# Kernel tuning notes

Hardware: AMD Instinct MI355X
Metric: run time of the kernel (lower is better)

## Reference

```python
import jax, jax.numpy as jnp
import numpy as np

HEADS = 8
HEAD_DIM = 64
WINDOW = 65  # odd


def setup_inputs() -> dict:
    key = jax.random.key(0)
    k1, k2, k3 = jax.random.split(key, 3)
    B, S, D_MODEL = 2, 2048, HEADS * HEAD_DIM
    x = jax.random.normal(k1, (B, S, D_MODEL), dtype=jnp.float32)
    W_qkv = jax.random.normal(k2, (D_MODEL, 3 * HEADS * HEAD_DIM), dtype=jnp.float32) * (1.0 / np.sqrt(D_MODEL))
    W_out = jax.random.normal(k3, (HEADS * HEAD_DIM, D_MODEL), dtype=jnp.float32) * (1.0 / np.sqrt(HEADS * HEAD_DIM))
    b_out = jnp.zeros((D_MODEL,), dtype=jnp.float32)
    return {"x": x, "W_qkv": W_qkv, "W_out": W_out, "b_out": b_out}


def reference(x, W_qkv, W_out, b_out):
    B, S, _ = x.shape
    H, D, W = HEADS, HEAD_DIM, WINDOW
    pad = W // 2

    qkv = x @ W_qkv                              # [B,S,3*H*D]
    qkv = qkv.reshape(B, S, H, 3 * D)
    q, k, v = jnp.split(qkv, 3, axis=-1)          # each [B,S,H,D]

    # zero-pad along sequence (matches tf.pad; padded keys get score 0, NOT -inf)
    k_pad = jnp.pad(k, ((0, 0), (pad, pad), (0, 0), (0, 0)))
    v_pad = jnp.pad(v, ((0, 0), (pad, pad), (0, 0), (0, 0)))

    # sliding windows via gather: [S, W] indices into padded seq (= tf.signal.frame)
    idx = jnp.arange(S)[:, None] + jnp.arange(W)[None, :]
    k_win = k_pad[:, idx]                         # [B,S,W,H,D]
    v_win = v_pad[:, idx]                         # [B,S,W,H,D]

    scale = 1.0 / jnp.sqrt(jnp.asarray(D, dtype=x.dtype))
    scores = jnp.einsum('bshd,bswhd->bhsw', q, k_win) * scale  # [B,H,S,W]
    weights = jax.nn.softmax(scores, axis=-1)
    attn = jnp.einsum('bhsw,bswhd->bshd', weights, v_win)       # [B,S,H,D]
    attn = attn.reshape(B, S, H * D)
    return attn @ W_out + b_out
```

## Files before the change

### kernel.cpp

```cpp
#include <hip/hip_runtime.h>
#include <hip/hip_bf16.h>
#include <stdint.h>

typedef short short8 __attribute__((ext_vector_type(8)));
typedef float f32x4 __attribute__((ext_vector_type(4)));
typedef unsigned short ushort4_t __attribute__((ext_vector_type(4)));
typedef unsigned short ushort8_t __attribute__((ext_vector_type(8)));

#define S_LEN 2048
#define NQKV 1536
#define DMODEL 512

__device__ inline unsigned short f2bf(float f) {
  unsigned int u = __float_as_uint(f);
  unsigned int r = (u + 0x7FFFu + ((u >> 16) & 1u)) >> 16;
  return (unsigned short)r;
}

__device__ __forceinline__ void gll16(const unsigned short* g, unsigned short* l) {
  __builtin_amdgcn_global_load_lds(
      (const __attribute__((address_space(1))) unsigned int*)g,
      (__attribute__((address_space(3))) unsigned int*)l, 16, 0, 0);
}

__global__ __launch_bounds__(256) void k_prep(const float* __restrict__ x,
                                              unsigned short* __restrict__ xb,
                                              const float* __restrict__ w1,
                                              unsigned short* __restrict__ o1,
                                              const float* __restrict__ w2,
                                              unsigned short* __restrict__ o2,
                                              unsigned short* __restrict__ Kp,
                                              unsigned short* __restrict__ Vp) {
  __shared__ float T[32][33];
  int bid = blockIdx.x;
  int t = threadIdx.x;
  if (bid < 1024) {
    int i = (bid * 256 + t) * 8;
    float4 a = *(const float4*)(x + i);
    float4 b = *(const float4*)(x + i + 4);
    ushort8_t o;
    o[0] = f2bf(a.x); o[1] = f2bf(a.y); o[2] = f2bf(a.z); o[3] = f2bf(a.w);
    o[4] = f2bf(b.x); o[5] = f2bf(b.y); o[6] = f2bf(b.z); o[7] = f2bf(b.w);
    *(ushort8_t*)(xb + i) = o;
    return;
  }
  if (bid >= 2048) {
    int p = bid - 2048;
    ushort8_t z = {};
    if (p < 16) {
      unsigned short* dst = Kp + (size_t)p * 2112 * 64;
#pragma unroll
      for (int i = 0; i < 2; i++) {
        int s = t + 256 * i;
        int row = s >> 3, c = s & 7;
        int r2 = row < 32 ? row : row - 32 + 2080;
        *(ushort8_t*)&dst[r2 * 64 + c * 8] = z;
      }
    } else {
      unsigned short* dst = Vp + (size_t)(p - 16) * 64 * 2112;
#pragma unroll
      for (int i = 0; i < 2; i++) {
        int s = t + 256 * i;
        int d = s >> 3, side = (s >> 2) & 1, c = s & 3;
        *(ushort8_t*)&dst[(size_t)d * 2112 + side * 2080 + c * 8] = z;
      }
    }
    return;
  }
  bid -= 1024;
  int bx = bid & 63, byy = bid >> 6;
  const float* w; unsigned short* o; int cols;
  if (bx < 48) { w = w1; o = o1; cols = 1536; }
  else         { w = w2; o = o2; cols = 512; bx -= 48; }
  int r0 = byy * 32, c0 = bx * 32;
  int tr = t / 32, tc = t % 32;
#pragma unroll
  for (int i = 0; i < 4; i++) {
    int r = tr + i * 8;
    T[r][tc] = w[(size_t)(r0 + r) * cols + c0 + tc];
  }
  __syncthreads();
#pragma unroll
  for (int i = 0; i < 4; i++) {
    int rr = tr + i * 8;
    o[(size_t)(c0 + rr) * 512 + r0 + tc] = f2bf(T[tc][rr]);
  }
}

__global__ __launch_bounds__(128) void k_gemm1(const unsigned short* __restrict__ A,
                                               const unsigned short* __restrict__ Bt,
                                               unsigned short* __restrict__ qs,
                                               unsigned short* __restrict__ kp,
                                               unsigned short* __restrict__ vp) {
  __shared__ __align__(16) unsigned short smem[24576];
  const int ASZ = 128 * 64, BOFF = 2 * 128 * 64, BSZ = 64 * 64;
  const int t = threadIdx.x, lane = t & 63, wid = t >> 6;
  const int m0 = blockIdx.y * 128, n0 = blockIdx.x * 64;
  const int wm = wid * 64;
  const int lr = lane & 15, lg = lane >> 4;
  const unsigned short* Ab = A + (size_t)m0 * 512;
  const unsigned short* Bb = Bt + (size_t)n0 * 512;
  f32x4 acc[4][4] = {};

  auto stage = [&](int buf, int kt) {
#pragma unroll
    for (int c = 0; c < 8; c++) {
      int f = t + 128 * c;
      int row = f >> 3, ch = f & 7;
      gll16(Ab + (size_t)row * 512 + kt + ((ch ^ (row & 7)) << 3),
            &smem[buf * ASZ + f * 8]);
    }
#pragma unroll
    for (int c = 0; c < 4; c++) {
      int f = t + 128 * c;
      int row = f >> 3, ch = f & 7;
      gll16(Bb + (size_t)row * 512 + kt + ((ch ^ (row & 7)) << 3),
            &smem[BOFF + buf * BSZ + f * 8]);
    }
  };

  stage(0, 0);
  int buf = 0;
  for (int it = 0; it < 8; ++it) {
    __syncthreads();
    if (it + 1 < 8) stage(buf ^ 1, (it + 1) * 64);
    const unsigned short* Ap = &smem[buf * ASZ];
    const unsigned short* Bp = &smem[BOFF + buf * BSZ];
#pragma unroll
    for (int sl = 0; sl < 2; sl++) {
      const int cs = sl * 4 + lg;
      short8 af[4], bfv[4];
#pragma unroll
      for (int i = 0; i < 4; i++) {
        int row = wm + i * 16 + lr;
        af[i] = *(const short8*)&Ap[row * 64 + ((cs ^ (row & 7)) << 3)];
      }
#pragma unroll
      for (int i = 0; i < 4; i++) {
        int row = i * 16 + lr;
        bfv[i] = *(const short8*)&Bp[row * 64 + ((cs ^ (row & 7)) << 3)];
      }
#pragma unroll
      for (int mi = 0; mi < 4; mi++)
#pragma unroll
        for (int ni = 0; ni < 4; ni++)
          acc[mi][ni] = __builtin_amdgcn_mfma_f32_16x16x32_bf16(af[mi], bfv[ni], acc[mi][ni], 0, 0, 0);
    }
    buf ^= 1;
  }

  __syncthreads();
#pragma unroll
  for (int mi = 0; mi < 4; mi++)
#pragma unroll
    for (int ni = 0; ni < 4; ni++)
#pragma unroll
      for (int j = 0; j < 4; j++) {
        int row = wm + mi * 16 + lg * 4 + j;
        int col = ni * 16 + lr;
        smem[row * 64 + (((col >> 3) ^ ((row >> 3) & 7)) << 3) + (col & 7)] =
            f2bf(acc[mi][ni][j]);
      }
  __syncthreads();

  const int b_ = m0 >> 11;
  const int posb = m0 & 2047;
  const int h = n0 / 192, seg = (n0 % 192) >> 6;
  if (seg < 2) {
    unsigned short* dst = (seg == 0)
        ? qs + ((size_t)(b_ * 8 + h) * 2048 + posb) * 64
        : kp + ((size_t)(b_ * 8 + h) * 2112 + 32 + posb) * 64;
#pragma unroll
    for (int i = 0; i < 8; i++) {
      int s = t + 128 * i;
      int row = s >> 3, ch = s & 7;
      int src = row * 64 + ((ch ^ ((row >> 3) & 7)) << 3);
      *(ushort8_t*)&dst[s * 8] = *(const ushort8_t*)&smem[src];
    }
  } else {
    unsigned short* dst = vp + (size_t)(b_ * 8 + h) * 64 * 2112;
#pragma unroll
    for (int i = 0; i < 8; i++) {
      int s = t + 128 * i;
      int dl = s >> 4, pc = s & 15;
      ushort8_t v;
#pragma unroll
      for (int j = 0; j < 8; j++) {
        int row = pc * 8 + j;
        v[j] = smem[row * 64 + ((((dl >> 3) ^ (pc & 7)) << 3)) + (dl & 7)];
      }
      *(ushort8_t*)&dst[(size_t)dl * 2112 + 32 + posb + pc * 8] = v;
    }
  }
}

template <int BM, int BN>
__global__ __launch_bounds__(256) void k_gemm(const unsigned short* __restrict__ A,
                                              const unsigned short* __restrict__ Bt,
                                              float* __restrict__ Cout,
                                              const float* __restrict__ bias,
                                              int M, int N, int K) {
  constexpr int MR = BM / 32, NR = BN / 32;
  constexpr int CA = BM / 32, CB = BN / 32;
  constexpr int STAGE_SH = 2 * (BM + BN) * 64;
  constexpr int BOUNCE_SH = BM * BN * 2;
  constexpr int SMEM_SH = STAGE_SH > BOUNCE_SH ? STAGE_SH : BOUNCE_SH;
  __shared__ __align__(16) unsigned short smem[SMEM_SH];
  const int ASZ = BM * 64, BOFF = 2 * BM * 64, BSZ = BN * 64;

  const int t = threadIdx.x, lane = t & 63, wid = t >> 6;
  const int m0 = blockIdx.y * BM, n0 = blockIdx.x * BN;
  const int wm = (wid >> 1) * (BM / 2), wn = (wid & 1) * (BN / 2);
  const int lr = lane & 15, lg = lane >> 4;
  const unsigned short* Ab = A + (size_t)m0 * K;
  const unsigned short* Bb = Bt + (size_t)n0 * K;
  f32x4 acc[MR][NR] = {};

  const int NT = K / 64;
  auto stage = [&](int buf, int kt) {
#pragma unroll
    for (int c = 0; c < CA; c++) {
      int f = t + 256 * c;
      int row = f >> 3, ch = f & 7;
      gll16(Ab + (size_t)row * K + kt + ((ch ^ (row & 7)) << 3),
            &smem[buf * ASZ + f * 8]);
    }
#pragma unroll
    for (int c = 0; c < CB; c++) {
      int f = t + 256 * c;
      int row = f >> 3, ch = f & 7;
      gll16(Bb + (size_t)row * K + kt + ((ch ^ (row & 7)) << 3),
            &smem[BOFF + buf * BSZ + f * 8]);
    }
  };

  stage(0, 0);
  int buf = 0;
  for (int it = 0; it < NT; ++it) {
    __syncthreads();
    if (it + 1 < NT) stage(buf ^ 1, (it + 1) * 64);
    const unsigned short* Ap = &smem[buf * ASZ];
    const unsigned short* Bp = &smem[BOFF + buf * BSZ];
#pragma unroll
    for (int sl = 0; sl < 2; sl++) {
      const int cs = sl * 4 + lg;
      short8 af[MR], bfv[NR];
#pragma unroll
      for (int i = 0; i < MR; i++) {
        int row = wm + i * 16 + lr;
        af[i] = *(const short8*)&Ap[row * 64 + ((cs ^ (row & 7)) << 3)];
      }
#pragma unroll
      for (int i = 0; i < NR; i++) {
        int row = wn + i * 16 + lr;
        bfv[i] = *(const short8*)&Bp[row * 64 + ((cs ^ (row & 7)) << 3)];
      }
#pragma unroll
      for (int mi = 0; mi < MR; mi++)
#pragma unroll
        for (int ni = 0; ni < NR; ni++)
          acc[mi][ni] = __builtin_amdgcn_mfma_f32_16x16x32_bf16(af[mi], bfv[ni], acc[mi][ni], 0, 0, 0);
    }
    buf ^= 1;
  }

  __syncthreads();
  float* ft = (float*)smem;
#pragma unroll
  for (int mi = 0; mi < MR; mi++)
#pragma unroll
    for (int ni = 0; ni < NR; ni++)
#pragma unroll
      for (int j = 0; j < 4; j++)
        ft[(wm + mi * 16 + lg * 4 + j) * BN + wn + ni * 16 + lr] = acc[mi][ni][j];
  __syncthreads();
#pragma unroll
  for (int i = 0; i < BM * BN / 1024; i++) {
    int s = t + 256 * i;
    int row = s / (BN / 4), ch = s % (BN / 4);
    float4 v = *(const float4*)&ft[row * BN + ch * 4];
    float4 bv = *(const float4*)&bias[n0 + ch * 4];
    v.x += bv.x; v.y += bv.y; v.z += bv.z; v.w += bv.w;
    *(float4*)&Cout[(size_t)(m0 + row) * N + n0 + ch * 4] = v;
  }
}

__global__ __launch_bounds__(256) void k_attn(const unsigned short* __restrict__ Qs,
                                              const unsigned short* __restrict__ Kp,
                                              const unsigned short* __restrict__ Vp,
                                              unsigned short* __restrict__ attnb) {
  __shared__ __align__(16) unsigned short Kt[128 * 64];
  __shared__ __align__(16) unsigned short Vt[64 * 192];
  __shared__ __align__(16) unsigned short Qt[64 * 64];
  const int t = threadIdx.x, lane = t & 63, w = t >> 6;
  const int blk = blockIdx.x;
  const int sbi = blk & 31, h = (blk >> 5) & 7, b = blk >> 8;
  const int sb = sbi * 64;
  const int bh = b * 8 + h;
  const int lr = lane & 15, lg = lane >> 4;

  {
    const unsigned short* src = Kp + ((size_t)bh * 2112 + sb) * 64;
#pragma unroll
    for (int i = 0; i < 4; i++) {
      int s = t + 256 * i, row = s >> 3, c = s & 7;
      gll16(src + row * 64 + (c ^ (row & 7)) * 8, &Kt[s * 8]);
    }
  }
  {
    const unsigned short* src = Vp + (size_t)bh * 64 * 2112 + sb;
#pragma unroll
    for (int i = 0; i < 6; i++) {
      int s = t + 256 * i, d = s / 24, c = s - d * 24;
      gll16(src + (size_t)d * 2112 + (c ^ (d & 7)) * 8, &Vt[s * 8]);
    }
  }
  {
    const unsigned short* src = Qs + ((size_t)bh * 2048 + sb) * 64;
#pragma unroll
    for (int i = 0; i < 2; i++) {
      int s = t + 256 * i, row = s >> 3, c = s & 7;
      gll16(src + row * 64 + (c ^ (row & 7)) * 8, &Qt[s * 8]);
    }
  }
  __syncthreads();

  const int sw = (lr & 7) << 3;

  short8 qb[2];
#pragma unroll
  for (int ks = 0; ks < 2; ks++)
    qb[ks] = *(const short8*)&Qt[(w * 16 + lr) * 64 + ((ks * 32 + lg * 8) ^ sw)];

  f32x4 sc[5] = {};
#pragma unroll
  for (int ct = 0; ct < 5; ct++) {
#pragma unroll
    for (int ks = 0; ks < 2; ks++) {
      short8 ka = *(const short8*)&Kt[(w * 16 + ct * 16 + lr) * 64 + ((ks * 32 + lg * 8) ^ sw)];
      sc[ct] = __builtin_amdgcn_mfma_f32_16x16x32_bf16(ka, qb[ks], sc[ct], 0, 0, 0);
    }
  }

  float mx = -1e30f;
#pragma unroll
  for (int ct = 0; ct < 5; ct++)
#pragma unroll
    for (int j = 0; j < 4; j++) {
      int c2 = ct * 16 + lg * 4 + j;
      sc[ct][j] = (c2 >= lr && c2 <= lr + 64) ? sc[ct][j] * 0.125f : -1e30f;
      mx = fmaxf(mx, sc[ct][j]);
    }
  mx = fmaxf(mx, __shfl_xor(mx, 16, 64));
  mx = fmaxf(mx, __shfl_xor(mx, 32, 64));

  float pn[5][4];
  float sum = 0.0f;
#pragma unroll
  for (int ct = 0; ct < 5; ct++)
#pragma unroll
    for (int j = 0; j < 4; j++) {
      pn[ct][j] = __expf(sc[ct][j] - mx);
      sum += pn[ct][j];
    }
  sum += __shfl_xor(sum, 16, 64);
  sum += __shfl_xor(sum, 32, 64);
  float inv = 1.0f / sum;

  unsigned int w01[5], w23[5];
#pragma unroll
  for (int ct = 0; ct < 5; ct++) {
    w01[ct] = (unsigned int)f2bf(pn[ct][0] * inv) | ((unsigned int)f2bf(pn[ct][1] * inv) << 16);
    w23[ct] = (unsigned int)f2bf(pn[ct][2] * inv) | ((unsigned int)f2bf(pn[ct][3] * inv) << 16);
  }

  f32x4 oa[4] = {};
  const int h2 = lg & 1, tl = lg >> 1;
  const int sA = 32 * h2 + lr, sB = sA + 16;
#pragma unroll
  for (int ks = 0; ks < 3; ks++) {
    const int T0 = 2 * ks;
    const int T1 = (2 * ks + 1 < 5) ? (2 * ks + 1) : 4;
    unsigned int a0 = __shfl((int)w01[T0], sA, 64), a1 = __shfl((int)w23[T0], sA, 64);
    unsigned int a2 = __shfl((int)w01[T0], sB, 64), a3 = __shfl((int)w23[T0], sB, 64);
    unsigned int b0 = __shfl((int)w01[T1], sA, 64), b1 = __shfl((int)w23[T1], sA, 64);
    unsigned int b2 = __shfl((int)w01[T1], sB, 64), b3 = __shfl((int)w23[T1], sB, 64);
    union { unsigned int u[4]; short8 v; } pb;
    pb.u[0] = tl ? b0 : a0;
    pb.u[1] = tl ? b1 : a1;
    pb.u[2] = tl ? b2 : a2;
    pb.u[3] = tl ? b3 : a3;
    if (ks == 2 && tl) { pb.u[0] = 0; pb.u[1] = 0; pb.u[2] = 0; pb.u[3] = 0; }
    int pofl = w * 16 + ks * 32 + lg * 8;
#pragma unroll
    for (int nt = 0; nt < 4; nt++) {
      short8 va = *(const short8*)&Vt[(nt * 16 + lr) * 192 + (pofl ^ sw)];
      oa[nt] = __builtin_amdgcn_mfma_f32_16x16x32_bf16(va, pb.v, oa[nt], 0, 0, 0);
    }
  }

  const int s0 = sb + w * 16;
#pragma unroll
  for (int nt = 0; nt < 4; nt++) {
    ushort4_t o;
#pragma unroll
    for (int j = 0; j < 4; j++) o[j] = f2bf(oa[nt][j]);
    *(ushort4_t*)&attnb[((size_t)b * S_LEN + s0 + lr) * DMODEL + h * 64 + nt * 16 + lg * 4] = o;
  }
}

extern "C" void kernel_launch(void* const* d_in, const int* in_sizes, int n_in,
                              void* d_out, int out_size, void* d_ws, size_t ws_size,
                              hipStream_t stream) {
  const float* x    = (const float*)d_in[0];
  const float* Wqkv = (const float*)d_in[1];
  const float* Wout = (const float*)d_in[2];
  const float* bout = (const float*)d_in[3];
  char* ws = (char*)d_ws;
  unsigned short* xb    = (unsigned short*)(ws + 0);
  unsigned short* wqkvt = (unsigned short*)(ws + 4194304);
  unsigned short* woutt = (unsigned short*)(ws + 5767168);
  unsigned short* Qs    = (unsigned short*)(ws + 6291456);
  unsigned short* Kp    = (unsigned short*)(ws + 10485760);
  unsigned short* Vp    = (unsigned short*)(ws + 14811136);
  unsigned short* attnb = (unsigned short*)(ws + 19922944);

  hipLaunchKernelGGL(k_prep, dim3(2080), dim3(256), 0, stream,
                     x, xb, Wqkv, wqkvt, Wout, woutt, Kp, Vp);
  hipLaunchKernelGGL(k_gemm1, dim3(24, 32), dim3(128), 0, stream,
                     xb, wqkvt, Qs, Kp, Vp);
  hipLaunchKernelGGL(k_attn, dim3(512), dim3(256), 0, stream, Qs, Kp, Vp, attnb);
  hipLaunchKernelGGL((k_gemm<64, 64>), dim3(8, 64), dim3(256), 0, stream,
                     attnb, woutt, (float*)d_out, bout, 4096, 512, 512);
}
```

Baseline: 38.13 us.

## Fuse prep, QKV GEMM, attention and output GEMM into one cooperative kernel

Measured after the change: 145.5 us. 3.82x slower.

```diff
diff --git a/kernel.cpp b/kernel.cpp
--- a/kernel.cpp
+++ b/kernel.cpp
@@ -1,6 +1,9 @@
 #include <hip/hip_runtime.h>
 #include <hip/hip_bf16.h>
+#include <hip/hip_cooperative_groups.h>
 #include <stdint.h>
+
+namespace cg = cooperative_groups;
 
 typedef short short8 __attribute__((ext_vector_type(8)));
 typedef float f32x4 __attribute__((ext_vector_type(4)));
@@ -23,389 +26,396 @@
       (__attribute__((address_space(3))) unsigned int*)l, 16, 0, 0);
 }
 
-__global__ __launch_bounds__(256) void k_prep(const float* __restrict__ x,
-                                              unsigned short* __restrict__ xb,
-                                              const float* __restrict__ w1,
-                                              unsigned short* __restrict__ o1,
-                                              const float* __restrict__ w2,
-                                              unsigned short* __restrict__ o2,
-                                              unsigned short* __restrict__ Kp,
-                                              unsigned short* __restrict__ Vp) {
-  __shared__ float T[32][33];
-  int bid = blockIdx.x;
-  int t = threadIdx.x;
-  if (bid < 1024) {
-    int i = (bid * 256 + t) * 8;
-    float4 a = *(const float4*)(x + i);
-    float4 b = *(const float4*)(x + i + 4);
-    ushort8_t o;
-    o[0] = f2bf(a.x); o[1] = f2bf(a.y); o[2] = f2bf(a.z); o[3] = f2bf(a.w);
-    o[4] = f2bf(b.x); o[5] = f2bf(b.y); o[6] = f2bf(b.z); o[7] = f2bf(b.w);
-    *(ushort8_t*)(xb + i) = o;
-    return;
+__global__ __launch_bounds__(768, 3) void k_mega(
+    const float* __restrict__ x, const float* __restrict__ w1,
+    const float* __restrict__ w2, const float* __restrict__ bias,
+    unsigned short* __restrict__ xb, unsigned short* __restrict__ wqkvt,
+    unsigned short* __restrict__ woutt, unsigned short* __restrict__ Qs,
+    unsigned short* __restrict__ Kp, unsigned short* __restrict__ Vp,
+    unsigned short* __restrict__ attnb, float* __restrict__ out) {
+  __shared__ __align__(16) unsigned short smem[73728];
+  cg::grid_group grid = cg::this_grid();
+  const int blk = blockIdx.x;
+  const int t = threadIdx.x;
+  const int sub = t >> 8;
+  const int tl = t & 255;
+  const int lane = tl & 63, wid = tl >> 6;
+  const int lr = lane & 15, lg = lane >> 4;
+
+  {
+    float(*T)[33] = (float(*)[33])(smem + sub * 4096);
+    for (int it = 0; it < 3; ++it) {
+      int vb = blk * 3 + sub + it * 768;
+      int kind = (vb < 1024) ? 0 : (vb < 2048) ? 1 : (vb < 2080) ? 2 : -1;
+      const float* w = nullptr; unsigned short* o = nullptr;
+      int bx = 0, byy = 0, cols = 0;
+      if (kind == 0) {
+        int i = (vb * 256 + tl) * 8;
+        float4 a = *(const float4*)(x + i);
+        float4 b = *(const float4*)(x + i + 4);
+        ushort8_t ov;
+        ov[0] = f2bf(a.x); ov[1] = f2bf(a.y); ov[2] = f2bf(a.z); ov[3] = f2bf(a.w);
+        ov[4] = f2bf(b.x); ov[5] = f2bf(b.y); ov[6] = f2bf(b.z); ov[7] = f2bf(b.w);
+        *(ushort8_t*)(xb + i) = ov;
+      } else if (kind == 2) {
+        int p = vb - 2048;
+        ushort8_t z = {};
+        if (p < 16) {
+          unsigned short* dst = Kp + (size_t)p * 2112 * 64;
+#pragma unroll
+          for (int i = 0; i < 2; i++) {
+            int s = tl + 256 * i;
+            int row = s >> 3, c = s & 7;
+            int r2 = row < 32 ? row : row - 32 + 2080;
+            *(ushort8_t*)&dst[r2 * 64 + c * 8] = z;
+          }
+        } else {
+          unsigned short* dst = Vp + (size_t)(p - 16) * 64 * 2112;
+#pragma unroll
+          for (int i = 0; i < 2; i++) {
+            int s = tl + 256 * i;
+            int d = s >> 3, side = (s >> 2) & 1, c = s & 3;
+            *(ushort8_t*)&dst[(size_t)d * 2112 + side * 2080 + c * 8] = z;
+          }
+        }
+      } else if (kind == 1) {
+        int v2 = vb - 1024;
+        bx = v2 & 63; byy = v2 >> 6;
+        if (bx < 48) { w = w1; o = wqkvt; cols = 1536; }
+        else         { w = w2; o = woutt; cols = 512; bx -= 48; }
+        int r0 = byy * 32, c0 = bx * 32;
+        int tr = tl / 32, tc = tl % 32;
+#pragma unroll
+        for (int i = 0; i < 4; i++) {
+          int r = tr + i * 8;
+          T[r][tc] = w[(size_t)(r0 + r) * cols + c0 + tc];
+        }
+      }
+      __syncthreads();
+      if (kind == 1) {
+        int r0 = byy * 32, c0 = bx * 32;
+        int tr = tl / 32, tc = tl % 32;
+#pragma unroll
+        for (int i = 0; i < 4; i++) {
+          int rr = tr + i * 8;
+          o[(size_t)(c0 + rr) * 512 + r0 + tc] = f2bf(T[tc][rr]);
+        }
+      }
+      __syncthreads();
+    }
   }
-  if (bid >= 2048) {
-    int p = bid - 2048;
-    ushort8_t z = {};
-    if (p < 16) {
-      unsigned short* dst = Kp + (size_t)p * 2112 * 64;
+  grid.sync();
+
+  {
+    unsigned short* vs = smem + sub * 24576;
+    const int ASZ = 8192, BOFF = 16384, BSZ = 4096;
+    const int vb = blk * 3 + sub;
+    const int m0 = (vb / 24) * 128, n0 = (vb % 24) * 64;
+    const int wm = (wid >> 1) * 64, wn = (wid & 1) * 32;
+    const unsigned short* Ab = xb + (size_t)m0 * 512;
+    const unsigned short* Bb = wqkvt + (size_t)n0 * 512;
+    f32x4 acc[4][2] = {};
+
+    auto stage = [&](int buf, int kt) {
+#pragma unroll
+      for (int c = 0; c < 4; c++) {
+        int f = tl + 256 * c;
+        int row = f >> 3, ch = f & 7;
+        gll16(Ab + (size_t)row * 512 + kt + ((ch ^ (row & 7)) << 3),
+              &vs[buf * ASZ + f * 8]);
+      }
+#pragma unroll
+      for (int c = 0; c < 2; c++) {
+        int f = tl + 256 * c;
+        int row = f >> 3, ch = f & 7;
+        gll16(Bb + (size_t)row * 512 + kt + ((ch ^ (row & 7)) << 3),
+              &vs[BOFF + buf * BSZ + f * 8]);
+      }
+    };
+
+    stage(0, 0);
+    int buf = 0;
+    for (int it = 0; it < 8; ++it) {
+      __syncthreads();
+      if (it + 1 < 8) stage(buf ^ 1, (it + 1) * 64);
+      const unsigned short* Ap = &vs[buf * ASZ];
+      const unsigned short* Bp = &vs[BOFF + buf * BSZ];
+#pragma unroll
+      for (int sl = 0; sl < 2; sl++) {
+        const int cs = sl * 4 + lg;
+        short8 af[4], bfv[2];
+#pragma unroll
+        for (int i = 0; i < 4; i++) {
+          int row = wm + i * 16 + lr;
+          af[i] = *(const short8*)&Ap[row * 64 + ((cs ^ (row & 7)) << 3)];
+        }
+#pragma unroll
+        for (int i = 0; i < 2; i++) {
+          int row = wn + i * 16 + lr;
+          bfv[i] = *(const short8*)&Bp[row * 64 + ((cs ^ (row & 7)) << 3)];
+        }
+#pragma unroll
+        for (int mi = 0; mi < 4; mi++)
+#pragma unroll
+          for (int ni = 0; ni < 2; ni++)
+            acc[mi][ni] = __builtin_amdgcn_mfma_f32_16x16x32_bf16(af[mi], bfv[ni], acc[mi][ni], 0, 0, 0);
+      }
+      buf ^= 1;
+    }
+
+    __syncthreads();
+#pragma unroll
+    for (int mi = 0; mi < 4; mi++)
+#pragma unroll
+      for (int ni = 0; ni < 2; ni++)
+#pragma unroll
+        for (int j = 0; j < 4; j++) {
+          int row = wm + mi * 16 + lg * 4 + j;
+          int col = wn + ni * 16 + lr;
+          vs[row * 64 + (((col >> 3) ^ ((row >> 3) & 7)) << 3) + (col & 7)] =
+              f2bf(acc[mi][ni][j]);
+        }
+    __syncthreads();
+
+    const int b_ = m0 >> 11;
+    const int posb = m0 & 2047;
+    const int h = n0 / 192, seg = (n0 % 192) >> 6;
+    if (seg < 2) {
+      unsigned short* dst = (seg == 0)
+          ? Qs + ((size_t)(b_ * 8 + h) * 2048 + posb) * 64
+          : Kp + ((size_t)(b_ * 8 + h) * 2112 + 32 + posb) * 64;
+#pragma unroll
+      for (int i = 0; i < 4; i++) {
+        int s = tl + 256 * i;
+        int row = s >> 3, ch = s & 7;
+        int src = row * 64 + ((ch ^ ((row >> 3) & 7)) << 3);
+        *(ushort8_t*)&dst[s * 8] = *(const ushort8_t*)&vs[src];
+      }
+    } else {
+      unsigned short* dst = Vp + (size_t)(b_ * 8 + h) * 64 * 2112;
+#pragma unroll
+      for (int i = 0; i < 4; i++) {
+        int s = tl + 256 * i;
+        int dl = s >> 4, pc = s & 15;
+        ushort8_t v;
+#pragma unroll
+        for (int j = 0; j < 8; j++) {
+          int row = pc * 8 + j;
+          v[j] = vs[row * 64 + ((((dl >> 3) ^ (pc & 7)) << 3)) + (dl & 7)];
+        }
+        *(ushort8_t*)&dst[(size_t)dl * 2112 + 32 + posb + pc * 8] = v;
+      }
+    }
+  }
+  grid.sync();
+
+  {
+    unsigned short* Kt = smem;
+    unsigned short* Vt = smem + 12288;
+    unsigned short* Qt = smem + 28672;
+    const int h = blk & 7, sbi = (blk >> 3) & 15, b = blk >> 7;
+    const int sb = sbi * 128, bh = b * 8 + h;
+    const int w = t >> 6;
+    const int lane6 = t & 63;
+    const int alr = lane6 & 15, alg = lane6 >> 4;
+
+    {
+      const unsigned short* src = Kp + ((size_t)bh * 2112 + sb) * 64;
 #pragma unroll
       for (int i = 0; i < 2; i++) {
-        int s = t + 256 * i;
+        int s = t + 768 * i;
         int row = s >> 3, c = s & 7;
-        int r2 = row < 32 ? row : row - 32 + 2080;
-        *(ushort8_t*)&dst[r2 * 64 + c * 8] = z;
-      }
-    } else {
-      unsigned short* dst = Vp + (size_t)(p - 16) * 64 * 2112;
+        gll16(src + row * 64 + (c ^ (row & 7)) * 8, &Kt[s * 8]);
+      }
+    }
+    {
+      const unsigned short* src = Vp + (size_t)bh * 64 * 2112 + sb;
+#pragma unroll
+      for (int i = 0; i < 3; i++) {
+        int s = t + 768 * i;
+        if (s < 2048) {
+          int d = s >> 5, c = s & 31;
+          gll16(src + (size_t)d * 2112 + (c ^ (d & 7)) * 8, &Vt[s * 8]);
+        }
+      }
+    }
+    {
+      const unsigned short* src = Qs + ((size_t)bh * 2048 + sb) * 64;
 #pragma unroll
       for (int i = 0; i < 2; i++) {
-        int s = t + 256 * i;
-        int d = s >> 3, side = (s >> 2) & 1, c = s & 3;
-        *(ushort8_t*)&dst[(size_t)d * 2112 + side * 2080 + c * 8] = z;
-      }
-    }
-    return;
+        int s = t + 768 * i;
+        if (s < 1024) {
+          int row = s >> 3, c = s & 7;
+          gll16(src + row * 64 + (c ^ (row & 7)) * 8, &Qt[s * 8]);
+        }
+      }
+    }
+    __syncthreads();
+
+    if (w < 8) {
+      const int sw = (alr & 7) << 3;
+
+      short8 qb[2];
+#pragma unroll
+      for (int ks = 0; ks < 2; ks++)
+        qb[ks] = *(const short8*)&Qt[(w * 16 + alr) * 64 + ((ks * 32 + alg * 8) ^ sw)];
+
+      f32x4 sc[5] = {};
+#pragma unroll
+      for (int ct = 0; ct < 5; ct++) {
+#pragma unroll
+        for (int ks = 0; ks < 2; ks++) {
+          short8 ka = *(const short8*)&Kt[(w * 16 + ct * 16 + alr) * 64 + ((ks * 32 + alg * 8) ^ sw)];
+          sc[ct] = __builtin_amdgcn_mfma_f32_16x16x32_bf16(ka, qb[ks], sc[ct], 0, 0, 0);
+        }
+      }
+
+      float mx = -1e30f;
+#pragma unroll
+      for (int ct = 0; ct < 5; ct++)
+#pragma unroll
+        for (int j = 0; j < 4; j++) {
+          int c2 = ct * 16 + alg * 4 + j;
+          sc[ct][j] = (c2 >= alr && c2 <= alr + 64) ? sc[ct][j] * 0.125f : -1e30f;
+          mx = fmaxf(mx, sc[ct][j]);
+        }
+      mx = fmaxf(mx, __shfl_xor(mx, 16, 64));
+      mx = fmaxf(mx, __shfl_xor(mx, 32, 64));
+
+      float pn[5][4];
+      float sum = 0.0f;
+#pragma unroll
+      for (int ct = 0; ct < 5; ct++)
+#pragma unroll
+        for (int j = 0; j < 4; j++) {
+          pn[ct][j] = __expf(sc[ct][j] - mx);
+          sum += pn[ct][j];
+        }
+      sum += __shfl_xor(sum, 16, 64);
+      sum += __shfl_xor(sum, 32, 64);
+      float inv = 1.0f / sum;
+
+      unsigned int w01[5], w23[5];
+#pragma unroll
+      for (int ct = 0; ct < 5; ct++) {
+        w01[ct] = (unsigned int)f2bf(pn[ct][0] * inv) | ((unsigned int)f2bf(pn[ct][1] * inv) << 16);
+        w23[ct] = (unsigned int)f2bf(pn[ct][2] * inv) | ((unsigned int)f2bf(pn[ct][3] * inv) << 16);
+      }
+
+      f32x4 oa[4] = {};
+      const int h2 = alg & 1, tsel = alg >> 1;
+      const int sA = 32 * h2 + alr, sB = sA + 16;
+#pragma unroll
+      for (int ks = 0; ks < 3; ks++) {
+        const int T0 = 2 * ks;
+        const int T1 = (2 * ks + 1 < 5) ? (2 * ks + 1) : 4;
+        unsigned int a0 = __shfl((int)w01[T0], sA, 64), a1 = __shfl((int)w23[T0], sA, 64);
+        unsigned int a2 = __shfl((int)w01[T0], sB, 64), a3 = __shfl((int)w23[T0], sB, 64);
+        unsigned int b0 = __shfl((int)w01[T1], sA, 64), b1 = __shfl((int)w23[T1], sA, 64);
+        unsigned int b2 = __shfl((int)w01[T1], sB, 64), b3 = __shfl((int)w23[T1], sB, 64);
+        union { unsigned int u[4]; short8 v; } pb;
+        pb.u[0] = tsel ? b0 : a0;
+        pb.u[1] = tsel ? b1 : a1;
+        pb.u[2] = tsel ? b2 : a2;
+        pb.u[3] = tsel ? b3 : a3;
+        if (ks == 2 && tsel) { pb.u[0] = 0; pb.u[1] = 0; pb.u[2] = 0; pb.u[3] = 0; }
+        int pofl = w * 16 + ks * 32 + alg * 8;
+#pragma unroll
+        for (int nt = 0; nt < 4; nt++) {
+          short8 va = *(const short8*)&Vt[(nt * 16 + alr) * 256 + (pofl ^ sw)];
+          oa[nt] = __builtin_amdgcn_mfma_f32_16x16x32_bf16(va, pb.v, oa[nt], 0, 0, 0);
+        }
+      }
+
+      const int s0 = sb + w * 16;
+#pragma unroll
+      for (int nt = 0; nt < 4; nt++) {
+        ushort4_t o;
+#pragma unroll
+        for (int j = 0; j < 4; j++) o[j] = f2bf(oa[nt][j]);
+        *(ushort4_t*)&attnb[((size_t)b * S_LEN + s0 + alr) * DMODEL + h * 64 + nt * 16 + alg * 4] = o;
+      }
+    }
   }
-  bid -= 1024;
-  int bx = bid & 63, byy = bid >> 6;
-  const float* w; unsigned short* o; int cols;
-  if (bx < 48) { w = w1; o = o1; cols = 1536; }
-  else         { w = w2; o = o2; cols = 512; bx -= 48; }
-  int r0 = byy * 32, c0 = bx * 32;
-  int tr = t / 32, tc = t % 32;
-#pragma unroll
-  for (int i = 0; i < 4; i++) {
-    int r = tr + i * 8;
-    T[r][tc] = w[(size_t)(r0 + r) * cols + c0 + tc];
-  }
-  __syncthreads();
-#pragma unroll
-  for (int i = 0; i < 4; i++) {
-    int rr = tr + i * 8;
-    o[(size_t)(c0 + rr) * 512 + r0 + tc] = f2bf(T[tc][rr]);
-  }
-}
-
-__global__ __launch_bounds__(128) void k_gemm1(const unsigned short* __restrict__ A,
-                                               const unsigned short* __restrict__ Bt,
-                                               unsigned short* __restrict__ qs,
-                                               unsigned short* __restrict__ kp,
-                                               unsigned short* __restrict__ vp) {
-  __shared__ __align__(16) unsigned short smem[24576];
-  const int ASZ = 128 * 64, BOFF = 2 * 128 * 64, BSZ = 64 * 64;
-  const int t = threadIdx.x, lane = t & 63, wid = t >> 6;
-  const int m0 = blockIdx.y * 128, n0 = blockIdx.x * 64;
-  const int wm = wid * 64;
-  const int lr = lane & 15, lg = lane >> 4;
-  const unsigned short* Ab = A + (size_t)m0 * 512;
-  const unsigned short* Bb = Bt + (size_t)n0 * 512;
-  f32x4 acc[4][4] = {};
-
-  auto stage = [&](int buf, int kt) {
-#pragma unroll
-    for (int c = 0; c < 8; c++) {
-      int f = t + 128 * c;
-      int row = f >> 3, ch = f & 7;
-      gll16(Ab + (size_t)row * 512 + kt + ((ch ^ (row & 7)) << 3),
-            &smem[buf * ASZ + f * 8]);
-    }
-#pragma unroll
-    for (int c = 0; c < 4; c++) {
-      int f = t + 128 * c;
-      int row = f >> 3, ch = f & 7;
-      gll16(Bb + (size_t)row * 512 + kt + ((ch ^ (row & 7)) << 3),
-            &smem[BOFF + buf * BSZ + f * 8]);
-    }
-  };
-
-  stage(0, 0);
-  int buf = 0;
-  for (int it = 0; it < 8; ++it) {
+  grid.sync();
+
+  {
+    unsigned short* vs = smem + sub * 16384;
+    const int ASZ = 4096, BOFF = 8192, BSZ = 4096;
+    int vb = blk * 3 + sub;
+    int tile = vb < 512 ? vb : vb - 512;
+    const int m0 = (tile >> 3) * 64, n0 = (tile & 7) * 64;
+    const int wm = (wid >> 1) * 32, wn = (wid & 1) * 32;
+    const unsigned short* Ab = attnb + (size_t)m0 * 512;
+    const unsigned short* Bb = woutt + (size_t)n0 * 512;
+    f32x4 acc[2][2] = {};
+
+    auto stage = [&](int buf, int kt) {
+#pragma unroll
+      for (int c = 0; c < 2; c++) {
+        int f = tl + 256 * c;
+        int row = f >> 3, ch = f & 7;
+        gll16(Ab + (size_t)row * 512 + kt + ((ch ^ (row & 7)) << 3),
+              &vs[buf * ASZ + f * 8]);
+      }
+#pragma unroll
+      for (int c = 0; c < 2; c++) {
+        int f = tl + 256 * c;
+        int row = f >> 3, ch = f & 7;
+        gll16(Bb + (size_t)row * 512 + kt + ((ch ^ (row & 7)) << 3),
+              &vs[BOFF + buf * BSZ + f * 8]);
+      }
+    };
+
+    stage(0, 0);
+    int buf = 0;
+    for (int it = 0; it < 8; ++it) {
+      __syncthreads();
+      if (it + 1 < 8) stage(buf ^ 1, (it + 1) * 64);
+      const unsigned short* Ap = &vs[buf * ASZ];
+      const unsigned short* Bp = &vs[BOFF + buf * BSZ];
+#pragma unroll
+      for (int sl = 0; sl < 2; sl++) {
+        const int cs = sl * 4 + lg;
+        short8 af[2], bfv[2];
+#pragma unroll
+        for (int i = 0; i < 2; i++) {
+          int row = wm + i * 16 + lr;
+          af[i] = *(const short8*)&Ap[row * 64 + ((cs ^ (row & 7)) << 3)];
+        }
+#pragma unroll
+        for (int i = 0; i < 2; i++) {
+          int row = wn + i * 16 + lr;
+          bfv[i] = *(const short8*)&Bp[row * 64 + ((cs ^ (row & 7)) << 3)];
+        }
+#pragma unroll
+        for (int mi = 0; mi < 2; mi++)
+#pragma unroll
+          for (int ni = 0; ni < 2; ni++)
+            acc[mi][ni] = __builtin_amdgcn_mfma_f32_16x16x32_bf16(af[mi], bfv[ni], acc[mi][ni], 0, 0, 0);
+      }
+      buf ^= 1;
+    }
+
     __syncthreads();
-    if (it + 1 < 8) stage(buf ^ 1, (it + 1) * 64);
-    const unsigned short* Ap = &smem[buf * ASZ];
-    const unsigned short* Bp = &smem[BOFF + buf * BSZ];
-#pragma unroll
-    for (int sl = 0; sl < 2; sl++) {
-      const int cs = sl * 4 + lg;
-      short8 af[4], bfv[4];
-#pragma unroll
-      for (int i = 0; i < 4; i++) {
-        int row = wm + i * 16 + lr;
-        af[i] = *(const short8*)&Ap[row * 64 + ((cs ^ (row & 7)) << 3)];
-      }
-#pragma unroll
-      for (int i = 0; i < 4; i++) {
-        int row = i * 16 + lr;
-        bfv[i] = *(const short8*)&Bp[row * 64 + ((cs ^ (row & 7)) << 3)];
-      }
-#pragma unroll
-      for (int mi = 0; mi < 4; mi++)
-#pragma unroll
-        for (int ni = 0; ni < 4; ni++)
-          acc[mi][ni] = __builtin_amdgcn_mfma_f32_16x16x32_bf16(af[mi], bfv[ni], acc[mi][ni], 0, 0, 0);
-    }
-    buf ^= 1;
-  }
-
-  __syncthreads();
-#pragma unroll
-  for (int mi = 0; mi < 4; mi++)
-#pragma unroll
-    for (int ni = 0; ni < 4; ni++)
-#pragma unroll
-      for (int j = 0; j < 4; j++) {
-        int row = wm + mi * 16 + lg * 4 + j;
-        int col = ni * 16 + lr;
-        smem[row * 64 + (((col >> 3) ^ ((row >> 3) & 7)) << 3) + (col & 7)] =
-            f2bf(acc[mi][ni][j]);
-      }
-  __syncthreads();
-
-  const int b_ = m0 >> 11;
-  const int posb = m0 & 2047;
-  const int h = n0 / 192, seg = (n0 % 192) >> 6;
-  if (seg < 2) {
-    unsigned short* dst = (seg == 0)
-        ? qs + ((size_t)(b_ * 8 + h) * 2048 + posb) * 64
-        : kp + ((size_t)(b_ * 8 + h) * 2112 + 32 + posb) * 64;
-#pragma unroll
-    for (int i = 0; i < 8; i++) {
-      int s = t + 128 * i;
-      int row = s >> 3, ch = s & 7;
-      int src = row * 64 + ((ch ^ ((row >> 3) & 7)) << 3);
-      *(ushort8_t*)&dst[s * 8] = *(const ushort8_t*)&smem[src];
-    }
-  } else {
-    unsigned short* dst = vp + (size_t)(b_ * 8 + h) * 64 * 2112;
-#pragma unroll
-    for (int i = 0; i < 8; i++) {
-      int s = t + 128 * i;
-      int dl = s >> 4, pc = s & 15;
-      ushort8_t v;
-#pragma unroll
-      for (int j = 0; j < 8; j++) {
-        int row = pc * 8 + j;
-        v[j] = smem[row * 64 + ((((dl >> 3) ^ (pc & 7)) << 3)) + (dl & 7)];
-      }
-      *(ushort8_t*)&dst[(size_t)dl * 2112 + 32 + posb + pc * 8] = v;
-    }
-  }
-}
-
-template <int BM, int BN>
-__global__ __launch_bounds__(256) void k_gemm(const unsigned short* __restrict__ A,
-                                              const unsigned short* __restrict__ Bt,
-                                              float* __restrict__ Cout,
-                                              const float* __restrict__ bias,
-                                              int M, int N, int K) {
-  constexpr int MR = BM / 32, NR = BN / 32;
-  constexpr int CA = BM / 32, CB = BN / 32;
-  constexpr int STAGE_SH = 2 * (BM + BN) * 64;
-  constexpr int BOUNCE_SH = BM * BN * 2;
-  constexpr int SMEM_SH = STAGE_SH > BOUNCE_SH ? STAGE_SH : BOUNCE_SH;
-  __shared__ __align__(16) unsigned short smem[SMEM_SH];
-  const int ASZ = BM * 64, BOFF = 2 * BM * 64, BSZ = BN * 64;
-
-  const int t = threadIdx.x, lane = t & 63, wid = t >> 6;
-  const int m0 = blockIdx.y * BM, n0 = blockIdx.x * BN;
-  const int wm = (wid >> 1) * (BM / 2), wn = (wid & 1) * (BN / 2);
-  const int lr = lane & 15, lg = lane >> 4;
-  const unsigned short* Ab = A + (size_t)m0 * K;
-  const unsigned short* Bb = Bt + (size_t)n0 * K;
-  f32x4 acc[MR][NR] = {};
-
-  const int NT = K / 64;
-  auto stage = [&](int buf, int kt) {
-#pragma unroll
-    for (int c = 0; c < CA; c++) {
-      int f = t + 256 * c;
-      int row = f >> 3, ch = f & 7;
-      gll16(Ab + (size_t)row * K + kt + ((ch ^ (row & 7)) << 3),
-            &smem[buf * ASZ + f * 8]);
-    }
-#pragma unroll
-    for (int c = 0; c < CB; c++) {
-      int f = t + 256 * c;
-      int row = f >> 3, ch = f & 7;
-      gll16(Bb + (size_t)row * K + kt + ((ch ^ (row & 7)) << 3),
-            &smem[BOFF + buf * BSZ + f * 8]);
-    }
-  };
-
-  stage(0, 0);
-  int buf = 0;
-  for (int it = 0; it < NT; ++it) {
+    float* ft = (float*)vs;
+#pragma unroll
+    for (int mi = 0; mi < 2; mi++)
+#pragma unroll
+      for (int ni = 0; ni < 2; ni++)
+#pragma unroll
+        for (int j = 0; j < 4; j++)
+          ft[(wm + mi * 16 + lg * 4 + j) * 64 + wn + ni * 16 + lr] = acc[mi][ni][j];
     __syncthreads();
-    if (it + 1 < NT) stage(buf ^ 1, (it + 1) * 64);
-    const unsigned short* Ap = &smem[buf * ASZ];
-    const unsigned short* Bp = &smem[BOFF + buf * BSZ];
-#pragma unroll
-    for (int sl = 0; sl < 2; sl++) {
-      const int cs = sl * 4 + lg;
-      short8 af[MR], bfv[NR];
-#pragma unroll
-      for (int i = 0; i < MR; i++) {
-        int row = wm + i * 16 + lr;
-        af[i] = *(const short8*)&Ap[row * 64 + ((cs ^ (row & 7)) << 3)];
-      }
-#pragma unroll
-      for (int i = 0; i < NR; i++) {
-        int row = wn + i * 16 + lr;
-        bfv[i] = *(const short8*)&Bp[row * 64 + ((cs ^ (row & 7)) << 3)];
-      }
-#pragma unroll
-      for (int mi = 0; mi < MR; mi++)
-#pragma unroll
-        for (int ni = 0; ni < NR; ni++)
-          acc[mi][ni] = __builtin_amdgcn_mfma_f32_16x16x32_bf16(af[mi], bfv[ni], acc[mi][ni], 0, 0, 0);
-    }
-    buf ^= 1;
-  }
-
-  __syncthreads();
-  float* ft = (float*)smem;
-#pragma unroll
-  for (int mi = 0; mi < MR; mi++)
-#pragma unroll
-    for (int ni = 0; ni < NR; ni++)
-#pragma unroll
-      for (int j = 0; j < 4; j++)
-        ft[(wm + mi * 16 + lg * 4 + j) * BN + wn + ni * 16 + lr] = acc[mi][ni][j];
-  __syncthreads();
-#pragma unroll
-  for (int i = 0; i < BM * BN / 1024; i++) {
-    int s = t + 256 * i;
-    int row = s / (BN / 4), ch = s % (BN / 4);
-    float4 v = *(const float4*)&ft[row * BN + ch * 4];
-    float4 bv = *(const float4*)&bias[n0 + ch * 4];
-    v.x += bv.x; v.y += bv.y; v.z += bv.z; v.w += bv.w;
-    *(float4*)&Cout[(size_t)(m0 + row) * N + n0 + ch * 4] = v;
-  }
-}
-
-__global__ __launch_bounds__(256) void k_attn(const unsigned short* __restrict__ Qs,
-                                              const unsigned short* __restrict__ Kp,
-                                              const unsigned short* __restrict__ Vp,
-                                              unsigned short* __restrict__ attnb) {
-  __shared__ __align__(16) unsigned short Kt[128 * 64];
-  __shared__ __align__(16) unsigned short Vt[64 * 192];
-  __shared__ __align__(16) unsigned short Qt[64 * 64];
-  const int t = threadIdx.x, lane = t & 63, w = t >> 6;
-  const int blk = blockIdx.x;
-  const int sbi = blk & 31, h = (blk >> 5) & 7, b = blk >> 8;
-  const int sb = sbi * 64;
-  const int bh = b * 8 + h;
-  const int lr = lane & 15, lg = lane >> 4;
-
-  {
-    const unsigned short* src = Kp + ((size_t)bh * 2112 + sb) * 64;
 #pragma unroll
     for (int i = 0; i < 4; i++) {
-      int s = t + 256 * i, row = s >> 3, c = s & 7;
-      gll16(src + row * 64 + (c ^ (row & 7)) * 8, &Kt[s * 8]);
-    }
-  }
-  {
-    const unsigned short* src = Vp + (size_t)bh * 64 * 2112 + sb;
-#pragma unroll
-    for (int i = 0; i < 6; i++) {
-      int s = t + 256 * i, d = s / 24, c = s - d * 24;
-      gll16(src + (size_t)d * 2112 + (c ^ (d & 7)) * 8, &Vt[s * 8]);
-    }
-  }
-  {
-    const unsigned short* src = Qs + ((size_t)bh * 2048 + sb) * 64;
-#pragma unroll
-    for (int i = 0; i < 2; i++) {
-      int s = t + 256 * i, row = s >> 3, c = s & 7;
-      gll16(src + row * 64 + (c ^ (row & 7)) * 8, &Qt[s * 8]);
-    }
-  }
-  __syncthreads();
-
-  const int sw = (lr & 7) << 3;
-
-  short8 qb[2];
-#pragma unroll
-  for (int ks = 0; ks < 2; ks++)
-    qb[ks] = *(const short8*)&Qt[(w * 16 + lr) * 64 + ((ks * 32 + lg * 8) ^ sw)];
-
-  f32x4 sc[5] = {};
-#pragma unroll
-  for (int ct = 0; ct < 5; ct++) {
-#pragma unroll
-    for (int ks = 0; ks < 2; ks++) {
-      short8 ka = *(const short8*)&Kt[(w * 16 + ct * 16 + lr) * 64 + ((ks * 32 + lg * 8) ^ sw)];
-      sc[ct] = __builtin_amdgcn_mfma_f32_16x16x32_bf16(ka, qb[ks], sc[ct], 0, 0, 0);
-    }
-  }
-
-  float mx = -1e30f;
-#pragma unroll
-  for (int ct = 0; ct < 5; ct++)
-#pragma unroll
-    for (int j = 0; j < 4; j++) {
-      int c2 = ct * 16 + lg * 4 + j;
-      sc[ct][j] = (c2 >= lr && c2 <= lr + 64) ? sc[ct][j] * 0.125f : -1e30f;
-      mx = fmaxf(mx, sc[ct][j]);
-    }
-  mx = fmaxf(mx, __shfl_xor(mx, 16, 64));
-  mx = fmaxf(mx, __shfl_xor(mx, 32, 64));
-
-  float pn[5][4];
-  float sum = 0.0f;
-#pragma unroll
-  for (int ct = 0; ct < 5; ct++)
-#pragma unroll
-    for (int j = 0; j < 4; j++) {
-      pn[ct][j] = __expf(sc[ct][j] - mx);
-      sum += pn[ct][j];
-    }
-  sum += __shfl_xor(sum, 16, 64);
-  sum += __shfl_xor(sum, 32, 64);
-  float inv = 1.0f / sum;
-
-  unsigned int w01[5], w23[5];
-#pragma unroll
-  for (int ct = 0; ct < 5; ct++) {
-    w01[ct] = (unsigned int)f2bf(pn[ct][0] * inv) | ((unsigned int)f2bf(pn[ct][1] * inv) << 16);
-    w23[ct] = (unsigned int)f2bf(pn[ct][2] * inv) | ((unsigned int)f2bf(pn[ct][3] * inv) << 16);
-  }
-
-  f32x4 oa[4] = {};
-  const int h2 = lg & 1, tl = lg >> 1;
-  const int sA = 32 * h2 + lr, sB = sA + 16;
-#pragma unroll
-  for (int ks = 0; ks < 3; ks++) {
-    const int T0 = 2 * ks;
-    const int T1 = (2 * ks + 1 < 5) ? (2 * ks + 1) : 4;
-    unsigned int a0 = __shfl((int)w01[T0], sA, 64), a1 = __shfl((int)w23[T0], sA, 64);
-    unsigned int a2 = __shfl((int)w01[T0], sB, 64), a3 = __shfl((int)w23[T0], sB, 64);
-    unsigned int b0 = __shfl((int)w01[T1], sA, 64), b1 = __shfl((int)w23[T1], sA, 64);
-    unsigned int b2 = __shfl((int)w01[T1], sB, 64), b3 = __shfl((int)w23[T1], sB, 64);
-    union { unsigned int u[4]; short8 v; } pb;
-    pb.u[0] = tl ? b0 : a0;
-    pb.u[1] = tl ? b1 : a1;
-    pb.u[2] = tl ? b2 : a2;
-    pb.u[3] = tl ? b3 : a3;
-    if (ks == 2 && tl) { pb.u[0] = 0; pb.u[1] = 0; pb.u[2] = 0; pb.u[3] = 0; }
-    int pofl = w * 16 + ks * 32 + lg * 8;
-#pragma unroll
-    for (int nt = 0; nt < 4; nt++) {
-      short8 va = *(const short8*)&Vt[(nt * 16 + lr) * 192 + (pofl ^ sw)];
-      oa[nt] = __builtin_amdgcn_mfma_f32_16x16x32_bf16(va, pb.v, oa[nt], 0, 0, 0);
-    }
-  }
-
-  const int s0 = sb + w * 16;
-#pragma unroll
-  for (int nt = 0; nt < 4; nt++) {
-    ushort4_t o;
-#pragma unroll
-    for (int j = 0; j < 4; j++) o[j] = f2bf(oa[nt][j]);
-    *(ushort4_t*)&attnb[((size_t)b * S_LEN + s0 + lr) * DMODEL + h * 64 + nt * 16 + lg * 4] = o;
+      int s = tl + 256 * i;
+      int row = s >> 4, ch = s & 15;
+      float4 v = *(const float4*)&ft[row * 64 + ch * 4];
+      float4 bv = *(const float4*)&bias[n0 + ch * 4];
+      v.x += bv.x; v.y += bv.y; v.z += bv.z; v.w += bv.w;
+      *(float4*)&out[(size_t)(m0 + row) * DMODEL + n0 + ch * 4] = v;
+    }
   }
 }
 
@@ -424,12 +434,10 @@
   unsigned short* Kp    = (unsigned short*)(ws + 10485760);
   unsigned short* Vp    = (unsigned short*)(ws + 14811136);
   unsigned short* attnb = (unsigned short*)(ws + 19922944);
-
-  hipLaunchKernelGGL(k_prep, dim3(2080), dim3(256), 0, stream,
-                     x, xb, Wqkv, wqkvt, Wout, woutt, Kp, Vp);
-  hipLaunchKernelGGL(k_gemm1, dim3(24, 32), dim3(128), 0, stream,
-                     xb, wqkvt, Qs, Kp, Vp);
-  hipLaunchKernelGGL(k_attn, dim3(512), dim3(256), 0, stream, Qs, Kp, Vp, attnb);
-  hipLaunchKernelGGL((k_gemm<64, 64>), dim3(8, 64), dim3(256), 0, stream,
-                     attnb, woutt, (float*)d_out, bout, 4096, 512, 512);
+  float* out = (float*)d_out;
+
+  void* kargs[] = {(void*)&x, (void*)&Wqkv, (void*)&Wout, (void*)&bout,
+                   (void*)&xb, (void*)&wqkvt, (void*)&woutt, (void*)&Qs,
+                   (void*)&Kp, (void*)&Vp, (void*)&attnb, (void*)&out};
+  hipLaunchCooperativeKernel(k_mega, dim3(256), dim3(768), kargs, 0, stream);
 }
```
